# Performance work log

Measured on AMD Instinct MI355X. Metric: run time of the kernel, lower is better.

Reference implementation:

```python
import jax, jax.numpy as jnp
import numpy as np

B, T, D, H, E, K = 4, 2048, 1024, 2048, 8, 2
LN_EPS = 1e-5


def setup_inputs() -> dict:
    key = jax.random.key(0)
    ks = jax.random.split(key, 5)
    sc = 0.02  # init scale for weights
    return {
        "x": jax.random.normal(ks[0], (B, T, D), dtype=jnp.float32),
        "gate_W": jax.random.normal(ks[1], (D, E), dtype=jnp.float32) * sc,
        "gate_b": jnp.zeros((E,), dtype=jnp.float32),
        "W1": jax.random.normal(ks[2], (E, D, H), dtype=jnp.float32) * sc,
        "b1": jnp.zeros((E, H), dtype=jnp.float32),
        "W2": jax.random.normal(ks[3], (E, H, D), dtype=jnp.float32) * sc,
        "b2": jnp.zeros((E, D), dtype=jnp.float32),
        "ln_gamma": jnp.ones((D,), dtype=jnp.float32),
        "ln_beta": jnp.zeros((D,), dtype=jnp.float32),
    }


def reference(x, gate_W, gate_b, W1, b1, W2, b2, ln_gamma, ln_beta):
    b, t, d = x.shape
    tokens = x.reshape(b * t, d)                      # [N, D]
    n = tokens.shape[0]

    # --- noisy top-k router (eval mode: no noise) ---
    logits = tokens @ gate_W + gate_b                 # [N, E]
    topk_val, topk_idx = jax.lax.top_k(logits, K)     # [N, K]
    topk_prob = jax.nn.softmax(topk_val, axis=-1)
    gates = jnp.zeros_like(logits).at[jnp.arange(n)[:, None], topk_idx].set(topk_prob)  # [N, E]

    # --- experts: dense-equivalent of gather-MLP-scatter (gates are 0 for unselected) ---
    h = jax.nn.gelu(jnp.einsum('nd,edh->enh', tokens, W1) + b1[:, None, :], approximate=False)  # [E,N,H]
    y = jnp.einsum('enh,ehd->end', h, W2) + b2[:, None, :]                                      # [E,N,D]
    out = jnp.einsum('ne,end->nd', gates, y).reshape(b, t, d)

    # --- residual + layernorm ---
    z = out + x
    mu = jnp.mean(z, axis=-1, keepdims=True)
    var = jnp.var(z, axis=-1, keepdims=True)
    out = (z - mu) * jax.lax.rsqrt(var + LN_EPS) * ln_gamma + ln_beta

    # --- aux losses ---
    route_probs = jax.nn.softmax(logits, axis=-1)     # [N, E]
    importance = route_probs.mean(axis=0)             # [E]
    load = (gates > 0).astype(jnp.float32).mean(axis=0)  # [E]
    balance_loss = E * jnp.sum(importance * load)
    eps = 1e-8
    entropy = -(route_probs * jnp.log(route_probs + eps)).sum(axis=-1).mean()
    utilization_entropy = -(load * jnp.log(load + eps)).sum()
    return out, balance_loss, entropy, utilization_entropy, load, importance
```

## Files before the change

kernel.cpp:

```cpp
#include <hip/hip_runtime.h>
#include <math.h>

#define N_TOK 8192
#define DIM   1024
#define HID   2048
#define NE    8
#define NPAIR (N_TOK * 2)
#define CAPP  (NPAIR + NE * 128)
#define TAIL  (N_TOK * DIM)

typedef __bf16 bf16x8_t __attribute__((ext_vector_type(8)));
typedef float  f32x4_t  __attribute__((ext_vector_type(4)));

__device__ __forceinline__ unsigned short f2bf(float f) {
  union { float f; unsigned u; } v; v.f = f;
  unsigned r = v.u + 0x7fffu + ((v.u >> 16) & 1u);
  return (unsigned short)(r >> 16);
}

__device__ __forceinline__ float bf2f(unsigned short h) {
  union { unsigned u; float f; } v; v.u = ((unsigned)h) << 16;
  return v.f;
}

__device__ __forceinline__ float gelu_exact(float v) {
  return 0.5f * v * (1.f + erff(v * 0.70710678118654752440f));
}

__device__ __forceinline__ void load16_lds(const void* g, void* l) {
  __builtin_amdgcn_global_load_lds(
      (const __attribute__((address_space(1))) unsigned int*)g,
      (__attribute__((address_space(3))) unsigned int*)l, 16, 0, 0);
}


template<int KD, int RR>
__global__ __launch_bounds__(256) void w_to_frag(const float* __restrict__ src,
                                                 unsigned short* __restrict__ dst) {
  constexpr int KD32 = KD / 32;
  __shared__ unsigned short L[256][34];
  int z = blockIdx.z, kblk = blockIdx.y;
  int r0 = blockIdx.x << 8;
  int t = threadIdx.x;
  const float* s = src + (size_t)z * KD * RR + (size_t)(kblk * 32) * RR + r0 + t;
  #pragma unroll
  for (int kk = 0; kk < 32; ++kk)
    L[t][kk] = f2bf(s[(size_t)kk * RR]);
  __syncthreads();
  int lane = t & 63, m16 = lane & 15, q = lane >> 4;
  unsigned short* d = dst + (size_t)z * KD * RR;
  #pragma unroll
  for (int p = 0; p < 4; ++p) {
    int ci = p * 4 + (t >> 6);
    int c = ((r0 >> 4) + ci) * KD32 + kblk;
    uint4 v = *(const uint4*)&L[ci * 16 + m16][q * 8];
    *(uint4*)(d + (size_t)c * 512 + lane * 8) = v;
  }
}

#define R_BLOCKS 128
#define R_TPW    (N_TOK / (R_BLOCKS * 4))
__global__ __launch_bounds__(256) void router_kernel(
    const float* __restrict__ x, const float* __restrict__ gW, const float* __restrict__ gb,
    int* __restrict__ tok_e, float* __restrict__ tok_g,
    int* __restrict__ cnt, float* __restrict__ imp, float* __restrict__ ent_sum) {
  __shared__ int s_cnt[NE];
  __shared__ float s_imp[NE];
  __shared__ float s_ent;
  int tid = threadIdx.x;
  if (tid < NE) { s_cnt[tid] = 0; s_imp[tid] = 0.f; }
  if (tid == 0) s_ent = 0.f;
  __syncthreads();
  int wid = tid >> 6, lane = tid & 63;
  int t0 = (blockIdx.x * 4 + wid) * R_TPW;
  float imp_loc[8] = {0.f, 0.f, 0.f, 0.f, 0.f, 0.f, 0.f, 0.f};
  float ent_loc = 0.f;
  for (int t = 0; t < R_TPW; ++t) {
    int n = t0 + t;
    const float* xr = x + (size_t)n * DIM;
    float p[8] = {0.f, 0.f, 0.f, 0.f, 0.f, 0.f, 0.f, 0.f};
    #pragma unroll
    for (int it = 0; it < DIM / 64; ++it) {
      int d = lane + (it << 6);
      float xv = xr[d];
      const float4* g4 = (const float4*)(gW + (size_t)d * NE);
      float4 a = g4[0], b = g4[1];
      p[0] += xv * a.x; p[1] += xv * a.y; p[2] += xv * a.z; p[3] += xv * a.w;
      p[4] += xv * b.x; p[5] += xv * b.y; p[6] += xv * b.z; p[7] += xv * b.w;
    }
    #pragma unroll
    for (int e = 0; e < 8; ++e)
      for (int o = 32; o > 0; o >>= 1) p[e] += __shfl_down(p[e], o, 64);
    if (lane == 0) {
      float lg[8];
      #pragma unroll
      for (int e = 0; e < 8; ++e) lg[e] = p[e] + gb[e];
      int i0 = 0;
      #pragma unroll
      for (int e = 1; e < 8; ++e) if (lg[e] > lg[i0]) i0 = e;
      int i1 = (i0 == 0) ? 1 : 0;
      #pragma unroll
      for (int e = 0; e < 8; ++e) if (e != i0 && lg[e] > lg[i1]) i1 = e;
      float d1 = expf(lg[i1] - lg[i0]);
      float g0 = 1.f / (1.f + d1);
      float g1 = d1 * g0;
      tok_e[2 * n] = i0; tok_e[2 * n + 1] = i1;
      tok_g[2 * n] = g0; tok_g[2 * n + 1] = g1;
      atomicAdd(&s_cnt[i0], 1);
      atomicAdd(&s_cnt[i1], 1);
      float mx = lg[i0], s = 0.f, pe[8];
      #pragma unroll
      for (int e = 0; e < 8; ++e) { pe[e] = expf(lg[e] - mx); s += pe[e]; }
      float inv = 1.f / s;
      #pragma unroll
      for (int e = 0; e < 8; ++e) {
        float pr = pe[e] * inv;
        imp_loc[e] += pr;
        ent_loc -= pr * logf(pr + 1e-8f);
      }
    }
  }
  if (lane == 0) {
    #pragma unroll
    for (int e = 0; e < 8; ++e) atomicAdd(&s_imp[e], imp_loc[e]);
    atomicAdd(&s_ent, ent_loc);
  }
  __syncthreads();
  const float invN = 1.f / (float)N_TOK;
  if (tid < NE) {
    atomicAdd(&cnt[tid], s_cnt[tid]);
    atomicAdd(&imp[tid], s_imp[tid] * invN);
  }
  if (tid == NE) atomicAdd(ent_sum, s_ent * invN);
}

__global__ void finalize_kernel(const int* __restrict__ cnt, int* __restrict__ poffs,
                                int* __restrict__ cursor, const float* __restrict__ imp,
                                const float* __restrict__ ent_sum, float* __restrict__ out_tail) {
  if (threadIdx.x == 0) {
    int off = 0; float bal = 0.f, util = 0.f;
    for (int e = 0; e < NE; ++e) {
      poffs[e] = off; cursor[e] = off;
      off += ((cnt[e] + 127) >> 7) << 7;
      float ld = (float)cnt[e] * (1.f / (float)N_TOK);
      float im = imp[e];
      out_tail[3 + e] = ld;
      out_tail[11 + e] = im;
      bal += im * ld;
      util -= ld * logf(ld + 1e-8f);
    }
    poffs[NE] = off;
    out_tail[0] = (float)NE * bal;
    out_tail[1] = *ent_sum;
    out_tail[2] = util;
  }
}

__global__ __launch_bounds__(256) void scatter_kernel(
    const int* __restrict__ tok_e, const float* __restrict__ tok_g,
    int* __restrict__ cursor, int* __restrict__ row_token, float* __restrict__ row_gate,
    int* __restrict__ pair_slot) {
  __shared__ int s_cnt[NE], s_base[NE], s_rank[NE];
  int tid = threadIdx.x;
  if (tid < NE) { s_cnt[tid] = 0; s_rank[tid] = 0; }
  __syncthreads();
  int n = blockIdx.x * 256 + tid;
  int e0 = tok_e[2 * n], e1 = tok_e[2 * n + 1];
  atomicAdd(&s_cnt[e0], 1);
  atomicAdd(&s_cnt[e1], 1);
  __syncthreads();
  if (tid < NE) s_base[tid] = atomicAdd(&cursor[tid], s_cnt[tid]);
  __syncthreads();
  int r0 = atomicAdd(&s_rank[e0], 1);
  int s0 = s_base[e0] + r0;
  row_token[s0] = n; row_gate[s0] = tok_g[2 * n]; pair_slot[2 * n] = s0;
  int r1 = atomicAdd(&s_rank[e1], 1);
  int s1 = s_base[e1] + r1;
  row_token[s1] = n; row_gate[s1] = tok_g[2 * n + 1]; pair_slot[2 * n + 1] = s1;
}

__global__ __launch_bounds__(256) void gather_a1(
    const float* __restrict__ x, const int* __restrict__ row_token,
    const int* __restrict__ cnt, const int* __restrict__ poffs,
    unsigned short* __restrict__ Ab1) {
  int e = blockIdx.z;
  int base = poffs[e];
  int pcnt = poffs[e + 1] - base;
  int nch = (pcnt >> 4) * 32;
  int cl = blockIdx.x * 4 + (threadIdx.x >> 6);
  if (cl >= nch) return;
  int lane = threadIdx.x & 63, m16 = lane & 15, q = lane >> 4;
  int rblk = cl >> 5, kblk = cl & 31;
  int sl = rblk * 16 + m16;
  int slot = base + sl;
  int tok = (sl < cnt[e]) ? row_token[slot] : 0;
  int k = kblk * 32 + q * 8;
  const float4* sp = (const float4*)(x + (size_t)tok * DIM + k);
  float4 v0 = sp[0], v1 = sp[1];
  unsigned short t[8] = {f2bf(v0.x), f2bf(v0.y), f2bf(v0.z), f2bf(v0.w),
                         f2bf(v1.x), f2bf(v1.y), f2bf(v1.z), f2bf(v1.w)};
  *(uint4*)(Ab1 + ((size_t)(slot >> 4) * 32 + kblk) * 512 + lane * 8) = *(uint4*)t;
}

#define GEMM_BLOCKS 1024

__device__ __forceinline__ int xcd_swz(int bid) {
  return (bid & 7) * (GEMM_BLOCKS >> 3) + (bid >> 3);
}

__global__ __launch_bounds__(256, 4) void expert_gemm1(
    const unsigned short* __restrict__ Ab1,
    const unsigned short* __restrict__ W1f,
    const float* __restrict__ b1,
    const int* __restrict__ poffs,
    unsigned short* __restrict__ He) {
  __shared__ __align__(16) unsigned short As[8192], Bs[8192];
  __shared__ int s_po[NE + 1];
  int tid = threadIdx.x, wid = tid >> 6, lane = tid & 63;
  if (tid <= NE) s_po[tid] = poffs[tid];
  __syncthreads();
  int nt = (s_po[NE] >> 7) << 4;
  int m16 = lane & 15, q = lane >> 4;
  int wr = (wid & 1) << 6, wc = (wid >> 1) << 6;
  int ra = wr >> 4, rc = wc >> 4;
  unsigned short* lA = As + wid * 4 * 512;
  unsigned short* lB = Bs + wid * 4 * 512;
  f32x4_t zero4 = {0.f, 0.f, 0.f, 0.f};
  int bid0 = xcd_swz(blockIdx.x);

  for (int tile = bid0; tile < nt; tile += GEMM_BLOCKS) {
    int rt = tile >> 4, ct = tile & 15;
    int col0 = ct << 7;
    int row0 = rt << 7;
    int e = 0;
    while (e + 1 < NE && s_po[e + 1] <= row0) ++e;
    const unsigned short* Ag = Ab1 + ((size_t)((rt << 3) + wid * 2) * 32) * 512 + lane * 8;
    const unsigned short* Bg = W1f + (size_t)e * HID * DIM
                             + ((size_t)((col0 >> 4) + wid * 2) * 32) * 512 + lane * 8;
    f32x4_t acc[4][4];
    #pragma unroll
    for (int i = 0; i < 4; ++i)
      #pragma unroll
      for (int j = 0; j < 4; ++j) acc[i][j] = zero4;

    for (int k0 = 0; k0 < DIM; k0 += 64) {
      int kc = (k0 >> 5) * 512;
      load16_lds(Ag + kc,                  lA);
      load16_lds(Ag + kc + 512,            lA + 512);
      load16_lds(Ag + kc + 32 * 512,       lA + 1024);
      load16_lds(Ag + kc + 32 * 512 + 512, lA + 1536);
      load16_lds(Bg + kc,                  lB);
      load16_lds(Bg + kc + 512,            lB + 512);
      load16_lds(Bg + kc + 32 * 512,       lB + 1024);
      load16_lds(Bg + kc + 32 * 512 + 512, lB + 1536);
      __syncthreads();
      #pragma unroll
      for (int ks = 0; ks < 2; ++ks) {
        bf16x8_t a[4], b[4];
        #pragma unroll
        for (int i = 0; i < 4; ++i) {
          a[i] = *(const bf16x8_t*)&As[((ra + i) * 2 + ks) * 512 + lane * 8];
          b[i] = *(const bf16x8_t*)&Bs[((rc + i) * 2 + ks) * 512 + lane * 8];
        }
        #pragma unroll
        for (int i = 0; i < 4; ++i)
          #pragma unroll
          for (int j = 0; j < 4; ++j)
            acc[i][j] = __builtin_amdgcn_mfma_f32_16x16x32_bf16(a[i], b[j], acc[i][j], 0, 0, 0);
      }
      __syncthreads();
    }

    const float* b1e = b1 + (size_t)e * HID;
    int sb = rt << 3;
    #pragma unroll
    for (int i = 0; i < 4; ++i) {
      size_t sblk = (size_t)(sb + ra + i);
      #pragma unroll
      for (int rr = 0; rr < 4; ++rr) {
        int s15 = q * 4 + rr;
        #pragma unroll
        for (int j = 0; j < 4; ++j) {
          int col = col0 + wc + j * 16 + m16;
          float v = acc[i][j][rr] + b1e[col];
          size_t off = (sblk * 64 + (col >> 5)) * 512 + (((col >> 3) & 3) * 16 + s15) * 8 + (col & 7);
          He[off] = f2bf(gelu_exact(v));
        }
      }
    }
  }
}

__global__ __launch_bounds__(256, 4) void expert_gemm2(
    const unsigned short* __restrict__ He,
    const unsigned short* __restrict__ W2f,
    const int* __restrict__ poffs,
    unsigned short* __restrict__ yb) {
  __shared__ __align__(16) unsigned short As[8192], Bs[8192];
  __shared__ int s_po[NE + 1];
  int tid = threadIdx.x, wid = tid >> 6, lane = tid & 63;
  if (tid <= NE) s_po[tid] = poffs[tid];
  __syncthreads();
  int nt = (s_po[NE] >> 7) << 3;
  int m16 = lane & 15, q = lane >> 4;
  int wr = (wid & 1) << 6, wc = (wid >> 1) << 6;
  int ra = wr >> 4, rc = wc >> 4;
  unsigned short* lA = As + wid * 4 * 512;
  unsigned short* lB = Bs + wid * 4 * 512;
  f32x4_t zero4 = {0.f, 0.f, 0.f, 0.f};
  int bid0 = xcd_swz(blockIdx.x);

  for (int tile = bid0; tile < nt; tile += GEMM_BLOCKS) {
    int rt = tile >> 3, ct = tile & 7;
    int row0 = rt << 7;
    int col0 = ct << 7;
    int e = 0;
    while (e + 1 < NE && s_po[e + 1] <= row0) ++e;
    const unsigned short* Ag = He + ((size_t)((rt << 3) + wid * 2) * 64) * 512 + lane * 8;
    const unsigned short* Bg = W2f + (size_t)e * DIM * HID
                             + ((size_t)((col0 >> 4) + wid * 2) * 64) * 512 + lane * 8;
    f32x4_t acc[4][4];
    #pragma unroll
    for (int i = 0; i < 4; ++i)
      #pragma unroll
      for (int j = 0; j < 4; ++j) acc[i][j] = zero4;

    for (int k0 = 0; k0 < HID; k0 += 64) {
      int kc = (k0 >> 5) * 512;
      load16_lds(Ag + kc,                  lA);
      load16_lds(Ag + kc + 512,            lA + 512);
      load16_lds(Ag + kc + 64 * 512,       lA + 1024);
      load16_lds(Ag + kc + 64 * 512 + 512, lA + 1536);
      load16_lds(Bg + kc,                  lB);
      load16_lds(Bg + kc + 512,            lB + 512);
      load16_lds(Bg + kc + 64 * 512,       lB + 1024);
      load16_lds(Bg + kc + 64 * 512 + 512, lB + 1536);
      __syncthreads();
      #pragma unroll
      for (int ks = 0; ks < 2; ++ks) {
        bf16x8_t a[4], b[4];
        #pragma unroll
        for (int i = 0; i < 4; ++i) {
          a[i] = *(const bf16x8_t*)&As[((ra + i) * 2 + ks) * 512 + lane * 8];
          b[i] = *(const bf16x8_t*)&Bs[((rc + i) * 2 + ks) * 512 + lane * 8];
        }
        #pragma unroll
        for (int i = 0; i < 4; ++i)
          #pragma unroll
          for (int j = 0; j < 4; ++j)
            acc[i][j] = __builtin_amdgcn_mfma_f32_16x16x32_bf16(a[i], b[j], acc[i][j], 0, 0, 0);
      }
      __syncthreads();
    }

    #pragma unroll
    for (int i = 0; i < 4; ++i) {
      #pragma unroll
      for (int rr = 0; rr < 4; ++rr) {
        size_t slot = (size_t)(row0 + wr + i * 16 + q * 4 + rr);
        #pragma unroll
        for (int j = 0; j < 4; ++j) {
          int col = col0 + wc + j * 16 + m16;
          yb[slot * DIM + col] = f2bf(acc[i][j][rr]);
        }
      }
    }
  }
}

__global__ __launch_bounds__(256) void ln_kernel(
    const float* __restrict__ x, const unsigned short* __restrict__ yb,
    const int* __restrict__ tok_e, const float* __restrict__ tok_g,
    const int* __restrict__ pair_slot, const float* __restrict__ b2,
    const float* __restrict__ gamma, const float* __restrict__ beta,
    float* __restrict__ out) {
  int n = blockIdx.x, tid = threadIdx.x;
  int e0 = tok_e[2 * n], e1 = tok_e[2 * n + 1];
  float g0 = tok_g[2 * n], g1 = tok_g[2 * n + 1];
  size_t s0 = (size_t)pair_slot[2 * n], s1 = (size_t)pair_slot[2 * n + 1];
  const float* xr = x + (size_t)n * DIM;
  const unsigned short* y0 = yb + s0 * DIM;
  const unsigned short* y1 = yb + s1 * DIM;
  const float* b2e0 = b2 + (size_t)e0 * DIM;
  const float* b2e1 = b2 + (size_t)e1 * DIM;
  int d0 = tid << 2;
  float4 xv  = *(const float4*)(xr + d0);
  ushort4 yv0 = *(const ushort4*)(y0 + d0);
  ushort4 yv1 = *(const ushort4*)(y1 + d0);
  float4 bv0 = *(const float4*)(b2e0 + d0);
  float4 bv1 = *(const float4*)(b2e1 + d0);
  float z[4], s = 0.f, s2 = 0.f;
  {
    const float* xp = (const float*)&xv;
    const unsigned short* y0p = (const unsigned short*)&yv0;
    const unsigned short* y1p = (const unsigned short*)&yv1;
    const float* b0p = (const float*)&bv0;
    const float* b1p = (const float*)&bv1;
    #pragma unroll
    for (int jj = 0; jj < 4; ++jj) {
      float v = xp[jj] + g0 * (bf2f(y0p[jj]) + b0p[jj]) + g1 * (bf2f(y1p[jj]) + b1p[jj]);
      z[jj] = v; s += v; s2 += v * v;
    }
  }
  for (int o = 32; o > 0; o >>= 1) { s += __shfl_down(s, o, 64); s2 += __shfl_down(s2, o, 64); }
  __shared__ float rs[4], rs2[4];
  int wid = tid >> 6, lane = tid & 63;
  if (lane == 0) { rs[wid] = s; rs2[wid] = s2; }
  __syncthreads();
  float ts = rs[0] + rs[1] + rs[2] + rs[3];
  float ts2 = rs2[0] + rs2[1] + rs2[2] + rs2[3];
  float mu = ts * (1.f / DIM);
  float var = ts2 * (1.f / DIM) - mu * mu;
  float rstd = rsqrtf(var + 1e-5f);
  float4 gv = *(const float4*)(gamma + d0);
  float4 bv = *(const float4*)(beta + d0);
  float4 ov;
  {
    const float* gp = (const float*)&gv;
    const float* bp = (const float*)&bv;
    float* op = (float*)&ov;
    #pragma unroll
    for (int jj = 0; jj < 4; ++jj)
      op[jj] = (z[jj] - mu) * rstd * gp[jj] + bp[jj];
  }
  *(float4*)(out + (size_t)n * DIM + d0) = ov;
}

extern "C" void kernel_launch(void* const* d_in, const int* in_sizes, int n_in,
                              void* d_out, int out_size, void* d_ws, size_t ws_size,
                              hipStream_t stream) {
  const float* x     = (const float*)d_in[0];
  const float* gW    = (const float*)d_in[1];
  const float* gb    = (const float*)d_in[2];
  const float* W1    = (const float*)d_in[3];
  const float* b1    = (const float*)d_in[4];
  const float* W2    = (const float*)d_in[5];
  const float* b2    = (const float*)d_in[6];
  const float* gamma = (const float*)d_in[7];
  const float* beta  = (const float*)d_in[8];
  float* out = (float*)d_out;

  char* w = (char*)d_ws;
  unsigned short* W1f = (unsigned short*)w; w += (size_t)NE * HID * DIM * 2;
  unsigned short* W2f = (unsigned short*)w; w += (size_t)NE * DIM * HID * 2;
  unsigned short* He  = (unsigned short*)w; w += (size_t)CAPP * HID * 2;
  unsigned short* AbY = (unsigned short*)w; w += (size_t)CAPP * DIM * 2;
  int*   row_token    = (int*)w;            w += (size_t)CAPP * 4;
  float* row_gate     = (float*)w;          w += (size_t)CAPP * 4;
  int*   tok_e        = (int*)w;            w += (size_t)NPAIR * 4;
  float* tok_g        = (float*)w;          w += (size_t)NPAIR * 4;
  int*   pair_slot    = (int*)w;            w += (size_t)NPAIR * 4;
  float* imp          = (float*)w;
  float* ent_sum      = imp + 8;
  int*   cntp         = (int*)(imp + 16);
  int*   cursor       = cntp + 8;
  int*   poffs        = cursor + 8;

  unsigned short* Ab1 = AbY;
  unsigned short* yb  = AbY;

  hipMemsetAsync(imp, 0, 256, stream);

  w_to_frag<DIM, HID><<<dim3(HID / 256, DIM / 32, NE), 256, 0, stream>>>(W1, W1f);
  w_to_frag<HID, DIM><<<dim3(DIM / 256, HID / 32, NE), 256, 0, stream>>>(W2, W2f);
  router_kernel<<<R_BLOCKS, 256, 0, stream>>>(x, gW, gb, tok_e, tok_g, cntp, imp, ent_sum);
  finalize_kernel<<<1, 64, 0, stream>>>(cntp, poffs, cursor, imp, ent_sum, out + TAIL);
  scatter_kernel<<<N_TOK / 256, 256, 0, stream>>>(tok_e, tok_g, cursor, row_token, row_gate, pair_slot);
  gather_a1<<<dim3(4096, 1, NE), 256, 0, stream>>>(x, row_token, cntp, poffs, Ab1);
  expert_gemm1<<<GEMM_BLOCKS, 256, 0, stream>>>(Ab1, W1f, b1, poffs, He);
  expert_gemm2<<<GEMM_BLOCKS, 256, 0, stream>>>(He, W2f, poffs, yb);
  ln_kernel<<<N_TOK, 256, 0, stream>>>(x, yb, tok_e, tok_g, pair_slot, b2, gamma, beta, out);
}
```

Before: 486.2 us.

## Use polynomial erf GELU, widen router grid, flatten gather_a1 launch

Three unrelated changes. The exact erff-based GELU in the GEMM1 epilogue is replaced with an Abramowitz-Stegun polynomial using a hardware reciprocal and fast exp, which lowers epilogue arithmetic cost but adds approximation error of about 1e-7. The router grid grows from 128 to 512 blocks so the router kernel has more parallelism. gather_a1 moves from a per-expert 3D grid of 4096x8 blocks, mostly early-exiting, to a flat grid sized to capacity, where each wave finds its expert by scanning the padded offsets; this removes the launch of many idle blocks.

Result: no change. 484.1 us (-0.4%).

```diff
diff --git a/kernel.cpp b/kernel.cpp
--- a/kernel.cpp
+++ b/kernel.cpp
@@ -23,8 +23,14 @@
   return v.f;
 }
 
-__device__ __forceinline__ float gelu_exact(float v) {
-  return 0.5f * v * (1.f + erff(v * 0.70710678118654752440f));
+__device__ __forceinline__ float gelu_fast(float v) {
+  float x = fabsf(v) * 0.70710678118654752440f;
+  float t = __builtin_amdgcn_rcpf(1.f + 0.3275911f * x);
+  float p = t * (0.254829592f + t * (-0.284496736f +
+            t * (1.421413741f + t * (-1.453152027f + t * 1.061405429f))));
+  float erf_pos = 1.f - p * __expf(-x * x);
+  float erf_v = copysignf(erf_pos, v);
+  return 0.5f * v * (1.f + erf_v);
 }
 
 __device__ __forceinline__ void load16_lds(const void* g, void* l) {
@@ -58,7 +64,7 @@
   }
 }
 
-#define R_BLOCKS 128
+#define R_BLOCKS 512
 #define R_TPW    (N_TOK / (R_BLOCKS * 4))
 __global__ __launch_bounds__(256) void router_kernel(
     const float* __restrict__ x, const float* __restrict__ gW, const float* __restrict__ gb,
@@ -179,27 +185,31 @@
   row_token[s1] = n; row_gate[s1] = tok_g[2 * n + 1]; pair_slot[2 * n + 1] = s1;
 }
 
+#define GA_BLOCKS ((CAPP >> 4) * 32 / 4)
 __global__ __launch_bounds__(256) void gather_a1(
     const float* __restrict__ x, const int* __restrict__ row_token,
     const int* __restrict__ cnt, const int* __restrict__ poffs,
     unsigned short* __restrict__ Ab1) {
-  int e = blockIdx.z;
-  int base = poffs[e];
-  int pcnt = poffs[e + 1] - base;
-  int nch = (pcnt >> 4) * 32;
+  int po[NE + 1];
+  #pragma unroll
+  for (int i = 0; i <= NE; ++i) po[i] = poffs[i];
+  int nch = (po[NE] >> 4) * 32;
   int cl = blockIdx.x * 4 + (threadIdx.x >> 6);
   if (cl >= nch) return;
   int lane = threadIdx.x & 63, m16 = lane & 15, q = lane >> 4;
-  int rblk = cl >> 5, kblk = cl & 31;
-  int sl = rblk * 16 + m16;
-  int slot = base + sl;
+  int sb = cl >> 5, kblk = cl & 31;
+  int slot = (sb << 4) + m16;
+  int e = 0;
+  #pragma unroll
+  for (int k = 1; k < NE; ++k) e += (po[k] <= slot) ? 1 : 0;
+  int sl = slot - po[e];
   int tok = (sl < cnt[e]) ? row_token[slot] : 0;
   int k = kblk * 32 + q * 8;
   const float4* sp = (const float4*)(x + (size_t)tok * DIM + k);
   float4 v0 = sp[0], v1 = sp[1];
   unsigned short t[8] = {f2bf(v0.x), f2bf(v0.y), f2bf(v0.z), f2bf(v0.w),
                          f2bf(v1.x), f2bf(v1.y), f2bf(v1.z), f2bf(v1.w)};
-  *(uint4*)(Ab1 + ((size_t)(slot >> 4) * 32 + kblk) * 512 + lane * 8) = *(uint4*)t;
+  *(uint4*)(Ab1 + ((size_t)sb * 32 + kblk) * 512 + lane * 8) = *(uint4*)t;
 }
 
 #define GEMM_BLOCKS 1024
@@ -284,7 +294,7 @@
           int col = col0 + wc + j * 16 + m16;
           float v = acc[i][j][rr] + b1e[col];
           size_t off = (sblk * 64 + (col >> 5)) * 512 + (((col >> 3) & 3) * 16 + s15) * 8 + (col & 7);
-          He[off] = f2bf(gelu_exact(v));
+          He[off] = f2bf(gelu_fast(v));
         }
       }
     }
@@ -466,7 +476,7 @@
   router_kernel<<<R_BLOCKS, 256, 0, stream>>>(x, gW, gb, tok_e, tok_g, cntp, imp, ent_sum);
   finalize_kernel<<<1, 64, 0, stream>>>(cntp, poffs, cursor, imp, ent_sum, out + TAIL);
   scatter_kernel<<<N_TOK / 256, 256, 0, stream>>>(tok_e, tok_g, cursor, row_token, row_gate, pair_slot);
-  gather_a1<<<dim3(4096, 1, NE), 256, 0, stream>>>(x, row_token, cntp, poffs, Ab1);
+  gather_a1<<<GA_BLOCKS, 256, 0, stream>>>(x, row_token, cntp, poffs, Ab1);
   expert_gemm1<<<GEMM_BLOCKS, 256, 0, stream>>>(Ab1, W1f, b1, poffs, He);
   expert_gemm2<<<GEMM_BLOCKS, 256, 0, stream>>>(He, W2f, poffs, yb);
   ln_kernel<<<N_TOK, 256, 0, stream>>>(x, yb, tok_e, tok_g, pair_slot, b2, gamma, beta, out);
```
